# Performance work log

Hardware: AMD Instinct MI355X
Metric: run time of the kernel (lower is better)

## Reference

```python
import jax, jax.numpy as jnp
import numpy as np

EPS = 1e-7
ALPHA, GAMMA = 1.0, 2.0
W_CLASS, W_BBOX, W_GIOU, W_CUT = 1.0, 5.0, 2.0, 3.0
FN_PENALTY = 10.0
N = 4194304


def setup_inputs() -> dict:
    key = jax.random.key(0)
    k = jax.random.split(key, 6)
    return {
        "pred_logits": jax.random.normal(k[0], (N, 4), dtype=jnp.float32),
        "target_labels": jax.random.randint(k[1], (N,), 0, 4, dtype=jnp.int64),
        "pred_boxes": jax.random.uniform(k[2], (N, 4), dtype=jnp.float32),
        "target_boxes": jax.random.uniform(k[3], (N, 4), dtype=jnp.float32),
        "cutting_logits": jax.random.normal(k[4], (N,), dtype=jnp.float32),
        "cutting_targets": (jax.random.uniform(k[5], (N,)) < 0.3).astype(jnp.float32),
    }


def _focal_loss(logits, labels):
    # F.cross_entropy per-sample, then focal reweighting
    logp = jax.nn.log_softmax(logits, axis=-1)
    ce = -jnp.take_along_axis(logp, labels[:, None], axis=-1)[:, 0]
    pt = jnp.exp(-ce)
    return jnp.mean(ALPHA * (1.0 - pt) ** GAMMA * ce)


def _validate_and_fix(boxes):
    # _validate_and_fix_boxes: clamp(min=0) for rows with x1>x2 or y1>y2
    invalid = (boxes[:, 0] > boxes[:, 2]) | (boxes[:, 1] > boxes[:, 3])
    boxes = jnp.where(invalid[:, None], jnp.maximum(boxes, 0.0), boxes)
    # _fix_invalid_boxes inside generalized_box_iou: x2>=x1+1e-6, y2>=y1+1e-6
    x1, y1, x2, y2 = boxes[:, 0], boxes[:, 1], boxes[:, 2], boxes[:, 3]
    x2 = jnp.maximum(x2, x1 + 1e-6)
    y2 = jnp.maximum(y2, y1 + 1e-6)
    return jnp.stack([x1, y1, x2, y2], axis=1)


def _giou_loss(pred_boxes, target_boxes):
    # Matched-pair GIoU: same math as diag(generalized_box_iou(p, t)),
    # computed elementwise instead of materializing the [N,N] matrix.
    b1 = _validate_and_fix(pred_boxes)
    b2 = _validate_and_fix(target_boxes)
    area1 = (b1[:, 2] - b1[:, 0]) * (b1[:, 3] - b1[:, 1])
    area2 = (b2[:, 2] - b2[:, 0]) * (b2[:, 3] - b2[:, 1])
    lt = jnp.maximum(b1[:, :2], b2[:, :2])
    rb = jnp.minimum(b1[:, 2:], b2[:, 2:])
    wh = jnp.maximum(rb - lt, 0.0)
    inter = wh[:, 0] * wh[:, 1]
    union = area1 + area2 - inter
    iou = inter / (union + EPS)
    lt_e = jnp.minimum(b1[:, :2], b2[:, :2])
    rb_e = jnp.maximum(b1[:, 2:], b2[:, 2:])
    wh_e = jnp.maximum(rb_e - lt_e, 0.0)
    enclosing = wh_e[:, 0] * wh_e[:, 1]
    giou = iou - (enclosing - union) / (enclosing + EPS)
    return jnp.mean(jnp.maximum(1.0 - giou, 0.0))


def _weighted_bce(logits, targets):
    # BCEWithLogits, stable form
    bce = jnp.maximum(logits, 0.0) - logits * targets + jnp.log1p(jnp.exp(-jnp.abs(logits)))
    probs = jax.nn.sigmoid(logits)
    fn_mask = (targets == 1.0) & (probs < 0.5)
    weights = jnp.where(fn_mask, FN_PENALTY, 1.0)
    return jnp.mean(bce * weights)


def reference(pred_logits, target_labels, pred_boxes, target_boxes, cutting_logits, cutting_targets):
    loss_class = jnp.maximum(_focal_loss(pred_logits, target_labels), 0.0)
    loss_bbox = jnp.maximum(jnp.mean(jnp.abs(pred_boxes - target_boxes)), 0.0)
    loss_giou = jnp.maximum(_giou_loss(pred_boxes, target_boxes), 0.0)
    loss_cutting = jnp.maximum(_weighted_bce(cutting_logits, cutting_targets), 0.0)
    total = (W_CLASS * loss_class + W_BBOX * loss_bbox
             + W_GIOU * loss_giou + W_CUT * loss_cutting)
    return total, loss_class, loss_bbox, loss_giou, loss_cutting
```

## Files before the change

### kernel.cpp

```cpp
#include <hip/hip_runtime.h>
#include <math.h>

#define EPS 1e-7f
#define FN_PENALTY 10.0f
#define BLOCK 256

typedef float vf4 __attribute__((ext_vector_type(4)));

__device__ __forceinline__ float4 ntload4f(const float4* p) {
    vf4 v = __builtin_nontemporal_load((const vf4*)p);
    float4 r; r.x = v.x; r.y = v.y; r.z = v.z; r.w = v.w;
    return r;
}
__device__ __forceinline__ int ntloadi(const int* p) {
    return __builtin_nontemporal_load(p);
}
__device__ __forceinline__ float ntloadf(const float* p) {
    return __builtin_nontemporal_load(p);
}

__device__ __forceinline__ float waveReduceSum(float v) {
    #pragma unroll
    for (int off = 32; off > 0; off >>= 1)
        v += __shfl_down(v, off, 64);
    return v;
}

__device__ __forceinline__ float4 validate_fix(float4 b) {
    bool invalid = (b.x > b.z) || (b.y > b.w);
    if (invalid) {
        b.x = fmaxf(b.x, 0.0f);
        b.y = fmaxf(b.y, 0.0f);
        b.z = fmaxf(b.z, 0.0f);
        b.w = fmaxf(b.w, 0.0f);
    }
    b.z = fmaxf(b.z, b.x + 1e-6f);
    b.w = fmaxf(b.w, b.y + 1e-6f);
    return b;
}

__device__ __forceinline__ void accum_row(
    float4 lg, int lbl, float4 pb, float4 tb, float cl, float ct,
    float& s_class, float& s_bbox, float& s_giou, float& s_cut)
{
    float l0 = lg.x, l1 = lg.y, l2 = lg.z, l3 = lg.w;
    float m = fmaxf(fmaxf(l0, l1), fmaxf(l2, l3));
    float e0 = __expf(l0 - m), e1 = __expf(l1 - m),
          e2 = __expf(l2 - m), e3 = __expf(l3 - m);
    float se = e0 + e1 + e2 + e3;
    lbl &= 3;
    float lsel = (lbl == 0) ? l0 : (lbl == 1) ? l1 : (lbl == 2) ? l2 : l3;
    float esel = (lbl == 0) ? e0 : (lbl == 1) ? e1 : (lbl == 2) ? e2 : e3;
    float ce = __logf(se) + m - lsel;
    float pt = esel * __builtin_amdgcn_rcpf(se);
    float om = 1.0f - pt;
    s_class += om * om * ce;

    s_bbox += fabsf(pb.x - tb.x) + fabsf(pb.y - tb.y)
            + fabsf(pb.z - tb.z) + fabsf(pb.w - tb.w);

    float4 b1 = validate_fix(pb);
    float4 b2 = validate_fix(tb);
    float area1 = (b1.z - b1.x) * (b1.w - b1.y);
    float area2 = (b2.z - b2.x) * (b2.w - b2.y);
    float ltx = fmaxf(b1.x, b2.x), lty = fmaxf(b1.y, b2.y);
    float rbx = fminf(b1.z, b2.z), rby = fminf(b1.w, b2.w);
    float iw = fmaxf(rbx - ltx, 0.0f), ih = fmaxf(rby - lty, 0.0f);
    float inter = iw * ih;
    float uni = area1 + area2 - inter;
    float iou = __fdividef(inter, uni + EPS);
    float ex1 = fminf(b1.x, b2.x), ey1 = fminf(b1.y, b2.y);
    float ex2 = fmaxf(b1.z, b2.z), ey2 = fmaxf(b1.w, b2.w);
    float ew = fmaxf(ex2 - ex1, 0.0f), eh = fmaxf(ey2 - ey1, 0.0f);
    float enc = ew * eh;
    float giou = iou - __fdividef(enc - uni, enc + EPS);
    s_giou += fmaxf(1.0f - giou, 0.0f);

    float bce = fmaxf(cl, 0.0f) - cl * ct + __logf(1.0f + __expf(-fabsf(cl)));
    float w = ((ct == 1.0f) && (cl < 0.0f)) ? FN_PENALTY : 1.0f;
    s_cut += bce * w;
}

__device__ __forceinline__ void block_reduce_store(
    float s_class, float s_bbox, float s_giou, float s_cut,
    float4* __restrict__ out_slot)
{
    s_class = waveReduceSum(s_class);
    s_bbox  = waveReduceSum(s_bbox);
    s_giou  = waveReduceSum(s_giou);
    s_cut   = waveReduceSum(s_cut);

    __shared__ float red[4][4];
    const int lane = threadIdx.x & 63;
    const int wave = threadIdx.x >> 6;
    if (lane == 0) {
        red[wave][0] = s_class;
        red[wave][1] = s_bbox;
        red[wave][2] = s_giou;
        red[wave][3] = s_cut;
    }
    __syncthreads();
    if (threadIdx.x == 0) {
        float4 r;
        r.x = red[0][0] + red[1][0] + red[2][0] + red[3][0];
        r.y = red[0][1] + red[1][1] + red[2][1] + red[3][1];
        r.z = red[0][2] + red[1][2] + red[2][2] + red[3][2];
        r.w = red[0][3] + red[1][3] + red[2][3] + red[3][3];
        *out_slot = r;
    }
}

__global__ __launch_bounds__(BLOCK) void loss_reduce(
    const float4* __restrict__ pred_logits,
    const int*    __restrict__ labels,
    const float4* __restrict__ pred_boxes,
    const float4* __restrict__ target_boxes,
    const float*  __restrict__ cut_logits,
    const float*  __restrict__ cut_targets,
    float4* __restrict__ block_out, int n)
{
    float s_class = 0.0f, s_bbox = 0.0f, s_giou = 0.0f, s_cut = 0.0f;
    const int stride  = gridDim.x * BLOCK;
    const int stride2 = stride * 2;
    int i = blockIdx.x * BLOCK + threadIdx.x;

    for (; i + stride < n; i += stride2) {
        const int j = i + stride;
        float4 lgA = ntload4f(&pred_logits[i]);
        float4 lgB = ntload4f(&pred_logits[j]);
        float4 pbA = ntload4f(&pred_boxes[i]);
        float4 pbB = ntload4f(&pred_boxes[j]);
        float4 tbA = ntload4f(&target_boxes[i]);
        float4 tbB = ntload4f(&target_boxes[j]);
        int    lbA = ntloadi(&labels[i]);
        int    lbB = ntloadi(&labels[j]);
        float  clA = ntloadf(&cut_logits[i]);
        float  clB = ntloadf(&cut_logits[j]);
        float  ctA = ntloadf(&cut_targets[i]);
        float  ctB = ntloadf(&cut_targets[j]);

        accum_row(lgA, lbA, pbA, tbA, clA, ctA, s_class, s_bbox, s_giou, s_cut);
        accum_row(lgB, lbB, pbB, tbB, clB, ctB, s_class, s_bbox, s_giou, s_cut);
    }
    if (i < n) {
        accum_row(ntload4f(&pred_logits[i]), ntloadi(&labels[i]),
                  ntload4f(&pred_boxes[i]), ntload4f(&target_boxes[i]),
                  ntloadf(&cut_logits[i]), ntloadf(&cut_targets[i]),
                  s_class, s_bbox, s_giou, s_cut);
    }

    block_reduce_store(s_class, s_bbox, s_giou, s_cut, &block_out[blockIdx.x]);
}

__global__ __launch_bounds__(BLOCK) void finalize_all(
    const float4* __restrict__ in, int n,
    float* __restrict__ out, float inv_n)
{
    float c = 0.0f, b = 0.0f, g = 0.0f, u = 0.0f;
    for (int i = threadIdx.x; i < n; i += BLOCK) {
        float4 r = in[i];
        c += r.x; b += r.y; g += r.z; u += r.w;
    }
    c = waveReduceSum(c);
    b = waveReduceSum(b);
    g = waveReduceSum(g);
    u = waveReduceSum(u);

    __shared__ float red[4][4];
    const int lane = threadIdx.x & 63;
    const int wave = threadIdx.x >> 6;
    if (lane == 0) {
        red[wave][0] = c;
        red[wave][1] = b;
        red[wave][2] = g;
        red[wave][3] = u;
    }
    __syncthreads();
    if (threadIdx.x == 0) {
        float tc = red[0][0] + red[1][0] + red[2][0] + red[3][0];
        float tb = red[0][1] + red[1][1] + red[2][1] + red[3][1];
        float tg = red[0][2] + red[1][2] + red[2][2] + red[3][2];
        float tu = red[0][3] + red[1][3] + red[2][3] + red[3][3];
        float lc   = fmaxf(tc * inv_n, 0.0f);
        float lb   = fmaxf(tb * inv_n * 0.25f, 0.0f);
        float lg   = fmaxf(tg * inv_n, 0.0f);
        float lcut = fmaxf(tu * inv_n, 0.0f);
        float total = 1.0f * lc + 5.0f * lb + 2.0f * lg + 3.0f * lcut;
        out[0] = total;
        out[1] = lc;
        out[2] = lb;
        out[3] = lg;
        out[4] = lcut;
    }
}

extern "C" void kernel_launch(void* const* d_in, const int* in_sizes, int n_in,
                              void* d_out, int out_size, void* d_ws, size_t ws_size,
                              hipStream_t stream) {
    const float4* pred_logits  = (const float4*)d_in[0];
    const int*    labels       = (const int*)d_in[1];
    const float4* pred_boxes   = (const float4*)d_in[2];
    const float4* target_boxes = (const float4*)d_in[3];
    const float*  cut_logits   = (const float*)d_in[4];
    const float*  cut_targets  = (const float*)d_in[5];
    float4* ws4 = (float4*)d_ws;
    float*  out = (float*)d_out;
    const int n = in_sizes[1];

    const int grid1 = 4096;
    float4* part1 = ws4;

    loss_reduce<<<grid1, BLOCK, 0, stream>>>(pred_logits, labels, pred_boxes,
                                             target_boxes, cut_logits, cut_targets,
                                             part1, n);
    finalize_all<<<1, BLOCK, 0, stream>>>(part1, grid1, out, 1.0f / (float)n);
}
```

Before: 213.4 us.

## Fuse final reduction into main kernel via last-block atomic ticket

Replaces the separate single-block finalize kernel with a last-block-done pattern: each block writes its partial, fences, and takes an atomic ticket, and the final block sums all partials and writes the outputs. The grid also shrinks from 4096 to 2048 blocks. This is meant to remove the second kernel launch and its gap, at the cost of a memset launch for the counter and per-block atomics/fences.

```diff
diff --git a/kernel.cpp b/kernel.cpp
--- a/kernel.cpp
+++ b/kernel.cpp
@@ -4,6 +4,7 @@
 #define EPS 1e-7f
 #define FN_PENALTY 10.0f
 #define BLOCK 256
+#define GRID1 2048
 
 typedef float vf4 __attribute__((ext_vector_type(4)));
 
@@ -81,43 +82,16 @@
     s_cut += bce * w;
 }
 
-__device__ __forceinline__ void block_reduce_store(
-    float s_class, float s_bbox, float s_giou, float s_cut,
-    float4* __restrict__ out_slot)
-{
-    s_class = waveReduceSum(s_class);
-    s_bbox  = waveReduceSum(s_bbox);
-    s_giou  = waveReduceSum(s_giou);
-    s_cut   = waveReduceSum(s_cut);
-
-    __shared__ float red[4][4];
-    const int lane = threadIdx.x & 63;
-    const int wave = threadIdx.x >> 6;
-    if (lane == 0) {
-        red[wave][0] = s_class;
-        red[wave][1] = s_bbox;
-        red[wave][2] = s_giou;
-        red[wave][3] = s_cut;
-    }
-    __syncthreads();
-    if (threadIdx.x == 0) {
-        float4 r;
-        r.x = red[0][0] + red[1][0] + red[2][0] + red[3][0];
-        r.y = red[0][1] + red[1][1] + red[2][1] + red[3][1];
-        r.z = red[0][2] + red[1][2] + red[2][2] + red[3][2];
-        r.w = red[0][3] + red[1][3] + red[2][3] + red[3][3];
-        *out_slot = r;
-    }
-}
-
-__global__ __launch_bounds__(BLOCK) void loss_reduce(
+__global__ __launch_bounds__(BLOCK) void loss_fused(
     const float4* __restrict__ pred_logits,
     const int*    __restrict__ labels,
     const float4* __restrict__ pred_boxes,
     const float4* __restrict__ target_boxes,
     const float*  __restrict__ cut_logits,
     const float*  __restrict__ cut_targets,
-    float4* __restrict__ block_out, int n)
+    float4* __restrict__ block_out,
+    unsigned int* __restrict__ counter,
+    int n, float* __restrict__ out, float inv_n)
 {
     float s_class = 0.0f, s_bbox = 0.0f, s_giou = 0.0f, s_cut = 0.0f;
     const int stride  = gridDim.x * BLOCK;
@@ -149,16 +123,41 @@
                   s_class, s_bbox, s_giou, s_cut);
     }
 
-    block_reduce_store(s_class, s_bbox, s_giou, s_cut, &block_out[blockIdx.x]);
-}
-
-__global__ __launch_bounds__(BLOCK) void finalize_all(
-    const float4* __restrict__ in, int n,
-    float* __restrict__ out, float inv_n)
-{
+    s_class = waveReduceSum(s_class);
+    s_bbox  = waveReduceSum(s_bbox);
+    s_giou  = waveReduceSum(s_giou);
+    s_cut   = waveReduceSum(s_cut);
+
+    __shared__ float red[4][4];
+    __shared__ int is_last_s;
+    const int lane = threadIdx.x & 63;
+    const int wave = threadIdx.x >> 6;
+    if (lane == 0) {
+        red[wave][0] = s_class;
+        red[wave][1] = s_bbox;
+        red[wave][2] = s_giou;
+        red[wave][3] = s_cut;
+    }
+    __syncthreads();
+    if (threadIdx.x == 0) {
+        float4 r;
+        r.x = red[0][0] + red[1][0] + red[2][0] + red[3][0];
+        r.y = red[0][1] + red[1][1] + red[2][1] + red[3][1];
+        r.z = red[0][2] + red[1][2] + red[2][2] + red[3][2];
+        r.w = red[0][3] + red[1][3] + red[2][3] + red[3][3];
+        block_out[blockIdx.x] = r;
+        __threadfence();
+        unsigned int ticket = atomicAdd(counter, 1u);
+        is_last_s = (ticket == gridDim.x - 1) ? 1 : 0;
+    }
+    __syncthreads();
+    if (is_last_s == 0) return;
+
+    __threadfence();
     float c = 0.0f, b = 0.0f, g = 0.0f, u = 0.0f;
-    for (int i = threadIdx.x; i < n; i += BLOCK) {
-        float4 r = in[i];
+    #pragma unroll
+    for (int k = 0; k < GRID1 / BLOCK; ++k) {
+        float4 r = block_out[threadIdx.x + k * BLOCK];
         c += r.x; b += r.y; g += r.z; u += r.w;
     }
     c = waveReduceSum(c);
@@ -166,21 +165,19 @@
     g = waveReduceSum(g);
     u = waveReduceSum(u);
 
-    __shared__ float red[4][4];
-    const int lane = threadIdx.x & 63;
-    const int wave = threadIdx.x >> 6;
+    __shared__ float red2[4][4];
     if (lane == 0) {
-        red[wave][0] = c;
-        red[wave][1] = b;
-        red[wave][2] = g;
-        red[wave][3] = u;
+        red2[wave][0] = c;
+        red2[wave][1] = b;
+        red2[wave][2] = g;
+        red2[wave][3] = u;
     }
     __syncthreads();
     if (threadIdx.x == 0) {
-        float tc = red[0][0] + red[1][0] + red[2][0] + red[3][0];
-        float tb = red[0][1] + red[1][1] + red[2][1] + red[3][1];
-        float tg = red[0][2] + red[1][2] + red[2][2] + red[3][2];
-        float tu = red[0][3] + red[1][3] + red[2][3] + red[3][3];
+        float tc = red2[0][0] + red2[1][0] + red2[2][0] + red2[3][0];
+        float tb = red2[0][1] + red2[1][1] + red2[2][1] + red2[3][1];
+        float tg = red2[0][2] + red2[1][2] + red2[2][2] + red2[3][2];
+        float tu = red2[0][3] + red2[1][3] + red2[2][3] + red2[3][3];
         float lc   = fmaxf(tc * inv_n, 0.0f);
         float lb   = fmaxf(tb * inv_n * 0.25f, 0.0f);
         float lg   = fmaxf(tg * inv_n, 0.0f);
@@ -203,15 +200,15 @@
     const float4* target_boxes = (const float4*)d_in[3];
     const float*  cut_logits   = (const float*)d_in[4];
     const float*  cut_targets  = (const float*)d_in[5];
-    float4* ws4 = (float4*)d_ws;
-    float*  out = (float*)d_out;
+    float4*       part1   = (float4*)d_ws;
+    unsigned int* counter = (unsigned int*)((char*)d_ws + GRID1 * sizeof(float4));
+    float*        out     = (float*)d_out;
     const int n = in_sizes[1];
-
-    const int grid1 = 4096;
-    float4* part1 = ws4;
-
-    loss_reduce<<<grid1, BLOCK, 0, stream>>>(pred_logits, labels, pred_boxes,
-                                             target_boxes, cut_logits, cut_targets,
-                                             part1, n);
-    finalize_all<<<1, BLOCK, 0, stream>>>(part1, grid1, out, 1.0f / (float)n);
-}
+    const float inv_n = 1.0f / (float)n;
+
+    hipMemsetAsync(counter, 0, sizeof(unsigned int), stream);
+
+    loss_fused<<<GRID1, BLOCK, 0, stream>>>(pred_logits, labels, pred_boxes,
+                                            target_boxes, cut_logits, cut_targets,
+                                            part1, counter, n, out, inv_n);
+}
```

Result: slower. 312.1 us (+46.3%).
